# Kernel tuning notes

Measured on AMD Instinct MI355X. Metric: run time of the kernel, lower is better.

Reference implementation:

```python
import jax, jax.numpy as jnp
import numpy as np

N = 100000      # nodes
E = 3200000     # edges (avg degree 32)
XD = 256        # x_dim
H = 128         # h_dim
G = 128         # g_dim
D = H + G + 1   # y_rep_dim


def setup_inputs() -> dict:
    key = jax.random.key(0)
    ks = jax.random.split(key, 16)
    s = 0.05
    f32 = jnp.float32
    return {
        "X": jax.random.normal(ks[0], (N, XD), f32),
        "T": jax.random.uniform(ks[1], (N,), f32),
        "edge_index": jax.random.randint(ks[2], (2, E), 0, N, dtype=jnp.int64),
        "W_phi": jax.random.normal(ks[3], (XD, H), f32) * s,
        "b_phi": jnp.zeros((H,), f32),
        "W_gcn": jax.random.normal(ks[4], (H, G), f32) * s,
        "b_gcn": jnp.zeros((G,), f32),
        "W00": jax.random.normal(ks[5], (D, D), f32) * s,
        "b00": jnp.zeros((D,), f32),
        "W10": jax.random.normal(ks[6], (D, D), f32) * s,
        "b10": jnp.zeros((D,), f32),
        "W01": jax.random.normal(ks[7], (D, 1), f32) * s,
        "b01": jnp.zeros((1,), f32),
        "W11": jax.random.normal(ks[8], (D, 1), f32) * s,
        "b11": jnp.zeros((1,), f32),
    }


def reference(X, T, edge_index, W_phi, b_phi, W_gcn, b_gcn,
              W00, b00, W10, b10, W01, b01, W11, b11):
    src = edge_index[0]  # row: message source
    dst = edge_index[1]  # col: message destination (adj_t aggregates into dst)

    # phi_x = ReLU(Linear(X))
    phi_x = jax.nn.relu(X @ W_phi + b_phi)          # [N, H]
    phi_x_t = T[:, None] * phi_x                    # [N, H]

    # GCNConv: linear -> symmetric-normalized aggregation with self loops
    h = phi_x_t @ W_gcn                             # [N, G]
    ones_e = jnp.ones((E,), h.dtype)
    deg = jax.ops.segment_sum(ones_e, dst, num_segments=N) + 1.0  # with self loop
    dis = jax.lax.rsqrt(deg)                        # deg^{-1/2}
    coef = (dis[src] * dis[dst])[:, None]           # per-edge norm
    msg = h[src] * coef                             # [E, G] gather
    agg = jax.ops.segment_sum(msg, dst, num_segments=N)           # scatter-sum
    agg = agg + h * (1.0 / deg)[:, None] + b_gcn    # self-loop term + bias
    rep_gnn = jax.nn.relu(agg)                      # dropout is identity in eval

    # z = scatter_sum(T over neighbors) / degree (no self loops)
    deg_nl = jax.ops.segment_sum(ones_e, dst, num_segments=N)
    z = jax.ops.segment_sum(T[src], dst, num_segments=N) / jnp.maximum(deg_nl, 1.0)

    rep_post = jnp.concatenate([phi_x, rep_gnn, z[:, None]], axis=1)  # [N, D]

    y00 = jax.nn.relu(rep_post @ W00 + b00)
    y10 = jax.nn.relu(rep_post @ W10 + b10)
    y0_pred = (y00 @ W01 + b01).reshape(-1)
    y1_pred = (y10 @ W11 + b11).reshape(-1)
    return (y0_pred, y1_pred, rep_post)
```

## Files before the change

kernel.cpp:

```cpp
#include <hip/hip_runtime.h>
#include <hip/hip_bf16.h>

#define NN 100000
#define EE 3200000
#define KXD 256
#define HH 128
#define GG 128
#define DD 257
#define ELLS 96

#define BNODES 128
#define NBKT 782
#define BCAP 4608
#define SCB 256
#define SCT 1024
#define EPB (EE / SCB)

#define NT 17
#define KT 9
#define KP 288
#define SROW 296

#define PKT 8
#define PNT 8
#define GKT 4
#define GNT 8

typedef __attribute__((ext_vector_type(8))) short short8;
typedef __attribute__((ext_vector_type(4))) float f32x4;
typedef __attribute__((ext_vector_type(4))) int i32x4;
typedef unsigned short ushort_t;

__device__ inline float bfu2f(unsigned short u) {
    return __uint_as_float(((unsigned int)u) << 16);
}
__device__ inline float ldf(const void* p, size_t i, int bf) {
    if (bf) return bfu2f(((const unsigned short*)p)[i]);
    return ((const float*)p)[i];
}
__device__ inline unsigned short f2bf(float v) {
    unsigned int u = __float_as_uint(v);
    return (unsigned short)((u + 0x7fff + ((u >> 16) & 1)) >> 16);
}

__global__ void k_probe(const int* __restrict__ ei32, const unsigned int* __restrict__ Xw,
                        int* __restrict__ flags)
{
    __shared__ int s_edge_any, s_bf_hits;
    const int t = threadIdx.x;
    if (t == 0) { s_edge_any = 0; s_bf_hits = 0; }
    __syncthreads();
    int acc = 0;
    #pragma unroll
    for (int j = 0; j < 64; ++j) {
        int k = (t + 256 * j) * 195;
        acc |= ei32[2 * (size_t)k + 1];
    }
    if (acc) atomicOr(&s_edge_any, 1);
    unsigned int lo = Xw[t] & 0xffffu;
    int e = (int)((lo >> 7) & 0xff);
    if (lo == 0u || (e >= 100 && e <= 140)) atomicAdd(&s_bf_hits, 1);
    __syncthreads();
    if (t == 0) {
        flags[0] = (s_edge_any == 0) ? 1 : 0;
        flags[1] = (s_bf_hits >= 192) ? 1 : 0;
    }
}

__device__ inline void edge_sd(const int* ei, int e, int i64, int& s, int& d) {
    if (i64) { s = ei[2 * (size_t)e]; d = ei[2 * ((size_t)EE + e)]; }
    else     { s = ei[e];             d = ei[(size_t)EE + e]; }
    s = min(max(s, 0), NN - 1);
    d = min(max(d, 0), NN - 1);
}
__device__ inline int edge_d(const int* ei, int e, int i64) {
    int d = i64 ? ei[2 * ((size_t)EE + e)] : ei[(size_t)EE + e];
    return min(max(d, 0), NN - 1);
}

__global__ __launch_bounds__(SCT) void k_scat(const int* __restrict__ ei,
    const int* __restrict__ flags, unsigned long long* __restrict__ ebuf,
    int* __restrict__ bcur)
{
    __shared__ int hist[NBKT];
    __shared__ int base[NBKT];
    const int t = threadIdx.x;
    for (int i = t; i < NBKT; i += SCT) hist[i] = 0;
    __syncthreads();
    const int i64 = flags[0];
    const int e0 = blockIdx.x * EPB;
    for (int e = e0 + t; e < e0 + EPB; e += SCT)
        atomicAdd(&hist[edge_d(ei, e, i64) >> 7], 1);
    __syncthreads();
    for (int bkt = t; bkt < NBKT; bkt += SCT) {
        int c = hist[bkt];
        base[bkt] = c ? atomicAdd(&bcur[bkt], c) : 0;
        hist[bkt] = 0;
    }
    __syncthreads();
    for (int e = e0 + t; e < e0 + EPB; e += SCT) {
        int s, d;
        edge_sd(ei, e, i64, s, d);
        int bkt = d >> 7;
        int r = atomicAdd(&hist[bkt], 1);
        int pos = base[bkt] + r;
        if (pos < BCAP) {
            unsigned long long v = ((unsigned long long)(unsigned)d << 32)
                                 | (unsigned long long)(unsigned)s;
            __builtin_nontemporal_store(v, &ebuf[(size_t)bkt * BCAP + pos]);
        }
    }
}

__global__ __launch_bounds__(256) void k_ell(const unsigned long long* __restrict__ ebuf,
    const int* __restrict__ bcur, const void* __restrict__ T,
    const int* __restrict__ flags,
    int* __restrict__ ell, int* __restrict__ deg, float* __restrict__ dis,
    float* __restrict__ z, float* __restrict__ out_rep)
{
    __shared__ int tile[BNODES][ELLS];
    __shared__ int cnt[BNODES];
    __shared__ float tsum[BNODES];
    const int t = threadIdx.x;
    const int b = blockIdx.x;
    const int n0 = b * BNODES;
    for (int i = t; i < BNODES; i += 256) { cnt[i] = 0; tsum[i] = 0.f; }
    __syncthreads();
    const int bf = flags[1];
    const int c = min(bcur[b], BCAP);
    const unsigned long long* __restrict__ reg = ebuf + (size_t)b * BCAP;
    for (int i = t; i < c; i += 256) {
        unsigned long long v = reg[i];
        int s  = (int)(v & 0xffffffffull);
        int dl = ((int)(v >> 32)) & (BNODES - 1);
        int slot = atomicAdd(&cnt[dl], 1);
        if (slot < ELLS) tile[dl][slot] = s;
        atomicAdd(&tsum[dl], fminf(fmaxf(ldf(T, s, bf), 0.f), 1.f));
    }
    __syncthreads();
    {
        const i32x4* src = (const i32x4*)&tile[0][0];
        i32x4* dst = (i32x4*)(ell + (size_t)n0 * ELLS);
        for (int i = t; i < BNODES * ELLS / 4; i += 256)
            __builtin_nontemporal_store(src[i], &dst[i]);
    }
    for (int i = t; i < BNODES; i += 256) {
        int n = n0 + i;
        if (n < NN) {
            int cN = cnt[i];
            float cf = (float)cN;
            deg[n] = cN;
            dis[n] = rsqrtf(cf + 1.f);
            float zv = tsum[i] / fmaxf(cf, 1.f);
            z[n] = zv;
            __builtin_nontemporal_store(zv, &out_rep[(size_t)n * DD + 256]);
        }
    }
}

__global__ __launch_bounds__(64) void k_packw(const void* __restrict__ W,
    const int* __restrict__ flags, unsigned short* __restrict__ Bp,
    int KTILES, int Ncols)
{
    const int blk = blockIdx.x;
    const int lane = threadIdx.x;
    const int nt = blk / KTILES, kt = blk - nt * KTILES;
    const int bf = flags[1];
    const int n = nt * 16 + (lane & 15);
    const int k0 = kt * 32 + (lane >> 4) * 8;
    unsigned short hi[8], lo[8];
    #pragma unroll
    for (int j = 0; j < 8; ++j) {
        float x = ldf(W, (size_t)(k0 + j) * Ncols + n, bf);
        hi[j] = f2bf(x);
        lo[j] = f2bf(x - bfu2f(hi[j]));
    }
    *(short8*)(Bp + ((size_t)blk * 2 + 0) * 512 + lane * 8) = *(short8*)hi;
    *(short8*)(Bp + ((size_t)blk * 2 + 1) * 512 + lane * 8) = *(short8*)lo;
}

__global__ __launch_bounds__(128) void k_phi(const void* __restrict__ X,
    const unsigned short* __restrict__ Bp, const void* __restrict__ b,
    const int* __restrict__ flags, float* __restrict__ phi,
    float* __restrict__ out_rep)
{
    const int t = threadIdx.x;
    const int wave = t >> 6, lane = t & 63;
    const int m = lane & 15, q = lane >> 4;
    const int row = blockIdx.x * 32 + wave * 16 + m;
    const int bf = flags[1];

    f32x4 acc[8];
    #pragma unroll
    for (int i = 0; i < 8; ++i) acc[i] = (f32x4){0.f, 0.f, 0.f, 0.f};

    for (int kt = 0; kt < PKT; ++kt) {
        short8 vah, vall;
        if (bf) {
            vah = *(const short8*)((const unsigned short*)X
                    + (size_t)row * KXD + kt * 32 + q * 8);
        } else {
            const float* xp = (const float*)X + (size_t)row * KXD + kt * 32 + q * 8;
            float4 u = *(const float4*)xp;
            float4 v = *(const float4*)(xp + 4);
            float xs[8] = {u.x, u.y, u.z, u.w, v.x, v.y, v.z, v.w};
            unsigned short ah[8], al[8];
            #pragma unroll
            for (int j = 0; j < 8; ++j) {
                ah[j] = f2bf(xs[j]);
                al[j] = f2bf(xs[j] - bfu2f(ah[j]));
            }
            vah = *(short8*)ah; vall = *(short8*)al;
        }
        const unsigned short* Bk = Bp + (size_t)kt * 1024 + lane * 8;
        if (bf) {
            #pragma unroll
            for (int nt = 0; nt < PNT; ++nt) {
                short8 bh = *(const short8*)(Bk + (size_t)nt * (PKT * 1024));
                acc[nt] = __builtin_amdgcn_mfma_f32_16x16x32_bf16(vah, bh, acc[nt], 0, 0, 0);
            }
        } else {
            #pragma unroll
            for (int nt = 0; nt < PNT; ++nt) {
                const unsigned short* bb = Bk + (size_t)nt * (PKT * 1024);
                short8 bh = *(const short8*)bb;
                short8 bl = *(const short8*)(bb + 512);
                acc[nt] = __builtin_amdgcn_mfma_f32_16x16x32_bf16(vah,  bh, acc[nt], 0, 0, 0);
                acc[nt] = __builtin_amdgcn_mfma_f32_16x16x32_bf16(vah,  bl, acc[nt], 0, 0, 0);
                acc[nt] = __builtin_amdgcn_mfma_f32_16x16x32_bf16(vall, bh, acc[nt], 0, 0, 0);
            }
        }
    }
    const int orow0 = blockIdx.x * 32 + wave * 16 + q * 4;
    #pragma unroll
    for (int nt = 0; nt < PNT; ++nt) {
        int col = nt * 16 + m;
        float bv = ldf(b, col, bf);
        #pragma unroll
        for (int r = 0; r < 4; ++r) {
            int orow = orow0 + r;
            float o = fmaxf(acc[nt][r] + bv, 0.f);
            phi[(size_t)orow * HH + col] = o;
            __builtin_nontemporal_store(o, &out_rep[(size_t)orow * DD + col]);
        }
    }
}

__global__ __launch_bounds__(128) void k_gcn(const float* __restrict__ phi,
    const void* __restrict__ T, const unsigned short* __restrict__ Bp,
    const float* __restrict__ dis, const int* __restrict__ flags,
    ushort_t* __restrict__ hs)
{
    const int t = threadIdx.x;
    const int wave = t >> 6, lane = t & 63;
    const int m = lane & 15, q = lane >> 4;
    const int row = blockIdx.x * 32 + wave * 16 + m;
    const int bf = flags[1];
    const float tv = ldf(T, row, bf);

    f32x4 acc[8];
    #pragma unroll
    for (int i = 0; i < 8; ++i) acc[i] = (f32x4){0.f, 0.f, 0.f, 0.f};

    for (int kt = 0; kt < GKT; ++kt) {
        const float* pp = phi + (size_t)row * HH + kt * 32 + q * 8;
        float4 u = *(const float4*)pp;
        float4 v = *(const float4*)(pp + 4);
        float xs[8] = {u.x, u.y, u.z, u.w, v.x, v.y, v.z, v.w};
        unsigned short ah[8], al[8];
        #pragma unroll
        for (int j = 0; j < 8; ++j) {
            float x = xs[j] * tv;
            ah[j] = f2bf(x);
            al[j] = f2bf(x - bfu2f(ah[j]));
        }
        short8 vah = *(short8*)ah, vall = *(short8*)al;
        const unsigned short* Bk = Bp + (size_t)kt * 1024 + lane * 8;
        #pragma unroll
        for (int nt = 0; nt < GNT; ++nt) {
            const unsigned short* bb = Bk + (size_t)nt * (GKT * 1024);
            short8 bh = *(const short8*)bb;
            short8 bl = *(const short8*)(bb + 512);
            acc[nt] = __builtin_amdgcn_mfma_f32_16x16x32_bf16(vah,  bh, acc[nt], 0, 0, 0);
            acc[nt] = __builtin_amdgcn_mfma_f32_16x16x32_bf16(vah,  bl, acc[nt], 0, 0, 0);
            acc[nt] = __builtin_amdgcn_mfma_f32_16x16x32_bf16(vall, bh, acc[nt], 0, 0, 0);
        }
    }
    const int orow0 = blockIdx.x * 32 + wave * 16 + q * 4;
    float dr[4];
    #pragma unroll
    for (int r = 0; r < 4; ++r) dr[r] = dis[orow0 + r];
    #pragma unroll
    for (int nt = 0; nt < GNT; ++nt) {
        int col = nt * 16 + m;
        #pragma unroll
        for (int r = 0; r < 4; ++r)
            hs[(size_t)(orow0 + r) * GG + col] = f2bf(acc[nt][r] * dr[r]);
    }
}

__global__ __launch_bounds__(256) void k_gather(const ushort_t* __restrict__ hs,
    const int* __restrict__ ell, const int* __restrict__ deg,
    const float* __restrict__ dis, const void* __restrict__ bg,
    const int* __restrict__ flags,
    ushort_t* __restrict__ repg_bf, float* __restrict__ out_rep)
{
    const int wv   = threadIdx.x >> 6;
    const int lane = threadIdx.x & 63;
    const int n    = blockIdx.x * 4 + wv;
    const int bf   = flags[1];
    const int c2   = lane * 2;
    const int dgc  = min(deg[n], ELLS);

    const ushort_t* __restrict__ hp = hs + c2;
    const int* __restrict__ er = ell + (size_t)n * ELLS;
    int v0 = er[lane];
    int v1 = er[64 + lane];

    float aL0=0.f,aL1=0.f,aL2=0.f,aL3=0.f;
    float aH0=0.f,aH1=0.f,aH2=0.f,aH3=0.f;

    const int m1 = min(dgc, 64);
    int j = 0;
    for (; j + 4 <= m1; j += 4) {
        int i0 = __builtin_amdgcn_readlane(v0, j);
        int i1 = __builtin_amdgcn_readlane(v0, j + 1);
        int i2 = __builtin_amdgcn_readlane(v0, j + 2);
        int i3 = __builtin_amdgcn_readlane(v0, j + 3);
        unsigned int p0 = *(const unsigned int*)(hp + ((size_t)i0 << 7));
        unsigned int p1 = *(const unsigned int*)(hp + ((size_t)i1 << 7));
        unsigned int p2 = *(const unsigned int*)(hp + ((size_t)i2 << 7));
        unsigned int p3 = *(const unsigned int*)(hp + ((size_t)i3 << 7));
        aL0 += __uint_as_float(p0 << 16);  aH0 += __uint_as_float(p0 & 0xffff0000u);
        aL1 += __uint_as_float(p1 << 16);  aH1 += __uint_as_float(p1 & 0xffff0000u);
        aL2 += __uint_as_float(p2 << 16);  aH2 += __uint_as_float(p2 & 0xffff0000u);
        aL3 += __uint_as_float(p3 << 16);  aH3 += __uint_as_float(p3 & 0xffff0000u);
    }
    for (; j < m1; ++j) {
        int i0 = __builtin_amdgcn_readlane(v0, j);
        unsigned int p0 = *(const unsigned int*)(hp + ((size_t)i0 << 7));
        aL0 += __uint_as_float(p0 << 16);  aH0 += __uint_as_float(p0 & 0xffff0000u);
    }
    for (; j < dgc; ++j) {
        int i0 = __builtin_amdgcn_readlane(v1, j - 64);
        unsigned int p0 = *(const unsigned int*)(hp + ((size_t)i0 << 7));
        aL0 += __uint_as_float(p0 << 16);  aH0 += __uint_as_float(p0 & 0xffff0000u);
    }
    float accL = (aL0 + aL1) + (aL2 + aL3);
    float accH = (aH0 + aH1) + (aH2 + aH3);

    unsigned int pn = *(const unsigned int*)(hp + ((size_t)n << 7));
    accL += __uint_as_float(pn << 16);
    accH += __uint_as_float(pn & 0xffff0000u);

    float dn = dis[n];
    float rL = fmaxf(fmaf(accL, dn, ldf(bg, c2, bf)), 0.f);
    float rH = fmaxf(fmaf(accH, dn, ldf(bg, c2 + 1, bf)), 0.f);

    unsigned int packed = (unsigned int)f2bf(rL) | ((unsigned int)f2bf(rH) << 16);
    *(unsigned int*)&repg_bf[(size_t)n * GG + c2] = packed;

    const size_t ob = (size_t)n * DD + HH + c2;
    __builtin_nontemporal_store(rL, &out_rep[ob]);
    __builtin_nontemporal_store(rH, &out_rep[ob + 1]);
}

__global__ __launch_bounds__(64) void k_pack(const void* W00, const void* b00,
    const void* W10, const void* b10, const int* __restrict__ flags,
    unsigned short* __restrict__ Bpk)
{
    const int blk  = blockIdx.x;
    const int lane = threadIdx.x;
    const int head = blk / (NT * KT);
    const int rem  = blk - head * NT * KT;
    const int nt   = rem / KT, kt = rem - (rem / KT) * KT;
    const void* WH = head ? W10 : W00;
    const void* bH = head ? b10 : b00;
    const int bf = flags[1];
    const int n  = nt * 16 + (lane & 15);
    const int k0 = kt * 32 + (lane >> 4) * 8;
    unsigned short v[8];
    #pragma unroll
    for (int j = 0; j < 8; ++j) {
        int k = k0 + j;
        float x = 0.f;
        if (n < DD) {
            if (k < DD)       x = ldf(WH, (size_t)k * DD + n, bf);
            else if (k == DD) x = ldf(bH, n, bf);
        }
        v[j] = f2bf(x);
    }
    *(short8*)(Bpk + ((size_t)blk * 64 + lane) * 8) = *(short8*)v;
}

__global__ __launch_bounds__(128) void k_heads_mfma(const float* __restrict__ phi,
    const ushort_t* __restrict__ repg_bf, const float* __restrict__ z,
    const unsigned short* __restrict__ Bpk,
    const void* W01, const void* b01, const void* W11, const void* b11,
    const int* __restrict__ flags, float* __restrict__ out)
{
    __shared__ unsigned short As[32][SROW];
    const int t = threadIdx.x;
    const int row0 = blockIdx.x * 32;
    const int bf = flags[1];

    for (int i = t; i < 32 * 16; i += 128) {
        int m = i >> 4, g = i & 15;
        const float* pp = &phi[(size_t)(row0 + m) * HH + g * 8];
        float4 u = *(const float4*)pp;
        float4 v = *(const float4*)(pp + 4);
        unsigned short w[8] = { f2bf(u.x), f2bf(u.y), f2bf(u.z), f2bf(u.w),
                                f2bf(v.x), f2bf(v.y), f2bf(v.z), f2bf(v.w) };
        *(short8*)&As[m][g * 8] = *(const short8*)w;
    }
    for (int i = t; i < 32 * 16; i += 128) {
        int m = i >> 4, g = i & 15;
        *(short8*)&As[m][HH + g * 8] =
            *(const short8*)&repg_bf[(size_t)(row0 + m) * GG + g * 8];
    }
    for (int i = t; i < 32 * 32; i += 128) {
        int m = i >> 5, k = 256 + (i & 31);
        unsigned short v = 0;
        if (k == 256)      v = f2bf(z[row0 + m]);
        else if (k == 257) v = 0x3F80;
        As[m][k] = v;
    }
    __syncthreads();

    const int wave = t >> 6;
    const int lane = t & 63;
    const int m = lane & 15, q = lane >> 4;

    const void* WV = wave ? W11 : W01;
    const float bV = ldf(wave ? b11 : b01, 0, bf);

    float r0[4] = {0.f, 0.f, 0.f, 0.f};
    float r1[4] = {0.f, 0.f, 0.f, 0.f};

    const unsigned short* Bh = Bpk + (size_t)wave * NT * KT * 64 * 8;
    for (int nt = 0; nt < NT; ++nt) {
        f32x4 acc0 = {0.f, 0.f, 0.f, 0.f};
        f32x4 acc1 = {0.f, 0.f, 0.f, 0.f};
        const unsigned short* Bn = Bh + (size_t)nt * KT * 64 * 8;
        #pragma unroll
        for (int kt = 0; kt < KT; ++kt) {
            short8 b  = *(const short8*)(Bn + ((size_t)kt * 64 + lane) * 8);
            short8 a0 = *(const short8*)&As[m][kt * 32 + q * 8];
            short8 a1 = *(const short8*)&As[m + 16][kt * 32 + q * 8];
            acc0 = __builtin_amdgcn_mfma_f32_16x16x32_bf16(a0, b, acc0, 0, 0, 0);
            acc1 = __builtin_amdgcn_mfma_f32_16x16x32_bf16(a1, b, acc1, 0, 0, 0);
        }
        int n = nt * 16 + m;
        float wv = (n < DD) ? ldf(WV, n, bf) : 0.f;
        #pragma unroll
        for (int r = 0; r < 4; ++r) {
            r0[r] += fmaxf(acc0[r], 0.f) * wv;
            r1[r] += fmaxf(acc1[r], 0.f) * wv;
        }
    }

    #pragma unroll
    for (int r = 0; r < 4; ++r) {
        #pragma unroll
        for (int off = 8; off > 0; off >>= 1) {
            r0[r] += __shfl_xor(r0[r], off);
            r1[r] += __shfl_xor(r1[r], off);
        }
    }
    if (m == 0) {
        #pragma unroll
        for (int r = 0; r < 4; ++r) {
            out[(size_t)wave * NN + row0 + q * 4 + r]      = r0[r] + bV;
            out[(size_t)wave * NN + row0 + 16 + q * 4 + r] = r1[r] + bV;
        }
    }
}

extern "C" void kernel_launch(void* const* d_in, const int* in_sizes, int n_in,
                              void* d_out, int out_size, void* d_ws, size_t ws_size,
                              hipStream_t stream)
{
    const void* X    = d_in[0];
    const void* T    = d_in[1];
    const int*  ei   = (const int*)d_in[2];
    const void* Wphi = d_in[3];
    const void* bphi = d_in[4];
    const void* Wgcn = d_in[5];
    const void* bgcn = d_in[6];
    const void* W00  = d_in[7];
    const void* b00  = d_in[8];
    const void* W10  = d_in[9];
    const void* b10  = d_in[10];
    const void* W01  = d_in[11];
    const void* b01  = d_in[12];
    const void* W11  = d_in[13];
    const void* b11  = d_in[14];
    float* out = (float*)d_out;
    float* out_rep = out + 2 * (size_t)NN;

    char* ws = (char*)d_ws;
    float*    phi   = (float*)ws;                         ws += (size_t)NN * HH * 4;
    ushort_t* hs    = (ushort_t*)ws;                      ws += (size_t)NN * GG * 2;
    ushort_t* repg  = (ushort_t*)ws;                      ws += (size_t)NN * GG * 2;
    int*      deg   = (int*)ws;                           ws += (size_t)NN * 4;
    float*    dis   = (float*)ws;                         ws += (size_t)NN * 4;
    float*    z     = (float*)ws;                         ws += (size_t)NN * 4;
    int*      ell   = (int*)ws;                           ws += (size_t)NBKT * BNODES * ELLS * 4;
    int*      flags = (int*)ws;                           ws += 16;
    int*      bcur  = (int*)ws;                           ws += (size_t)((NBKT + 15) & ~15) * 4;
    unsigned short* Bpk   = (unsigned short*)ws;          ws += (size_t)2 * NT * KT * 64 * 8 * 2;
    unsigned short* BpPhi = (unsigned short*)ws;          ws += (size_t)PNT * PKT * 2 * 512 * 2;
    unsigned short* BpGcn = (unsigned short*)ws;

    unsigned long long* ebuf = (unsigned long long*)phi;

    (void)hipMemsetAsync(bcur, 0, NBKT * sizeof(int), stream);

    k_probe <<<1,            256, 0, stream>>>(ei, (const unsigned int*)X, flags);
    k_scat  <<<SCB,          SCT, 0, stream>>>(ei, flags, ebuf, bcur);
    k_ell   <<<NBKT,         256, 0, stream>>>(ebuf, bcur, T, flags,
                                               ell, deg, dis, z, out_rep);
    k_pack  <<<2 * NT * KT,   64, 0, stream>>>(W00, b00, W10, b10, flags, Bpk);
    k_packw <<<PNT * PKT,     64, 0, stream>>>(Wphi, flags, BpPhi, PKT, HH);
    k_packw <<<GNT * GKT,     64, 0, stream>>>(Wgcn, flags, BpGcn, GKT, GG);
    k_phi   <<<NN / 32,      128, 0, stream>>>(X, BpPhi, bphi, flags, phi, out_rep);
    k_gcn   <<<NN / 32,      128, 0, stream>>>(phi, T, BpGcn, dis, flags, hs);
    k_gather<<<NN / 4,       256, 0, stream>>>(hs, ell, deg, dis, bgcn,
                                               flags, repg, out_rep);
    k_heads_mfma<<<NN / 32,  128, 0, stream>>>(phi, repg, z, Bpk,
                                               W01, b01, W11, b11, flags, out);
}
```

Before: 706.1 us.

## Stage edge bucketing in LDS and pack edges into 32-bit words

The scatter kernel now runs a block-wide prefix scan over bucket histograms and writes each edge into a bucket-sorted LDS staging array. It then writes to global memory in contiguous runs per bucket instead of scattered 8-byte stores. Each edge is packed as a 32-bit word holding the local destination in 7 bits and the source in 17 bits, which halves the edge buffer traffic that k_ell also reads. The cost is much more LDS per block (about 80KB with EPB=12500), an extra scan with many barriers, and a serial per-bucket fill loop.

```diff
diff --git a/kernel.cpp b/kernel.cpp
--- a/kernel.cpp
+++ b/kernel.cpp
@@ -79,40 +79,60 @@
 }
 
 __global__ __launch_bounds__(SCT) void k_scat(const int* __restrict__ ei,
-    const int* __restrict__ flags, unsigned long long* __restrict__ ebuf,
+    const int* __restrict__ flags, unsigned int* __restrict__ ebuf,
     int* __restrict__ bcur)
 {
     __shared__ int hist[NBKT];
+    __shared__ int loff[NBKT];
     __shared__ int base[NBKT];
+    __shared__ int hist2[NBKT];
+    __shared__ int sc[SCT];
+    __shared__ unsigned short bktof[EPB];
+    __shared__ unsigned int pk[EPB];
     const int t = threadIdx.x;
-    for (int i = t; i < NBKT; i += SCT) hist[i] = 0;
+    for (int i = t; i < NBKT; i += SCT) { hist[i] = 0; hist2[i] = 0; }
     __syncthreads();
     const int i64 = flags[0];
     const int e0 = blockIdx.x * EPB;
     for (int e = e0 + t; e < e0 + EPB; e += SCT)
         atomicAdd(&hist[edge_d(ei, e, i64) >> 7], 1);
     __syncthreads();
+    sc[t] = (t < NBKT) ? hist[t] : 0;
+    __syncthreads();
+    for (int off = 1; off < SCT; off <<= 1) {
+        int v = (t >= off) ? sc[t - off] : 0;
+        __syncthreads();
+        sc[t] += v;
+        __syncthreads();
+    }
+    if (t < NBKT) {
+        int c = hist[t];
+        loff[t] = sc[t] - c;
+        base[t] = c ? atomicAdd(&bcur[t], c) : 0;
+    }
+    __syncthreads();
     for (int bkt = t; bkt < NBKT; bkt += SCT) {
-        int c = hist[bkt];
-        base[bkt] = c ? atomicAdd(&bcur[bkt], c) : 0;
-        hist[bkt] = 0;
+        int st = loff[bkt], c = hist[bkt];
+        for (int j = 0; j < c; ++j) bktof[st + j] = (unsigned short)bkt;
     }
     __syncthreads();
     for (int e = e0 + t; e < e0 + EPB; e += SCT) {
         int s, d;
         edge_sd(ei, e, i64, s, d);
         int bkt = d >> 7;
-        int r = atomicAdd(&hist[bkt], 1);
-        int pos = base[bkt] + r;
-        if (pos < BCAP) {
-            unsigned long long v = ((unsigned long long)(unsigned)d << 32)
-                                 | (unsigned long long)(unsigned)s;
-            __builtin_nontemporal_store(v, &ebuf[(size_t)bkt * BCAP + pos]);
-        }
-    }
-}
-
-__global__ __launch_bounds__(256) void k_ell(const unsigned long long* __restrict__ ebuf,
+        int r = atomicAdd(&hist2[bkt], 1);
+        pk[loff[bkt] + r] = ((unsigned)(d & (BNODES - 1)) << 17) | (unsigned)s;
+    }
+    __syncthreads();
+    for (int i = t; i < EPB; i += SCT) {
+        int bkt = bktof[i];
+        int pos = base[bkt] + (i - loff[bkt]);
+        if (pos < BCAP)
+            __builtin_nontemporal_store(pk[i], &ebuf[(size_t)bkt * BCAP + pos]);
+    }
+}
+
+__global__ __launch_bounds__(256) void k_ell(const unsigned int* __restrict__ ebuf,
     const int* __restrict__ bcur, const void* __restrict__ T,
     const int* __restrict__ flags,
     int* __restrict__ ell, int* __restrict__ deg, float* __restrict__ dis,
@@ -128,11 +148,11 @@
     __syncthreads();
     const int bf = flags[1];
     const int c = min(bcur[b], BCAP);
-    const unsigned long long* __restrict__ reg = ebuf + (size_t)b * BCAP;
+    const unsigned int* __restrict__ reg = ebuf + (size_t)b * BCAP;
     for (int i = t; i < c; i += 256) {
-        unsigned long long v = reg[i];
-        int s  = (int)(v & 0xffffffffull);
-        int dl = ((int)(v >> 32)) & (BNODES - 1);
+        unsigned int v = reg[i];
+        int s  = (int)(v & 0x1FFFFu);
+        int dl = (int)(v >> 17) & (BNODES - 1);
         int slot = atomicAdd(&cnt[dl], 1);
         if (slot < ELLS) tile[dl][slot] = s;
         atomicAdd(&tsum[dl], fminf(fmaxf(ldf(T, s, bf), 0.f), 1.f));
@@ -512,7 +532,7 @@
     unsigned short* BpPhi = (unsigned short*)ws;          ws += (size_t)PNT * PKT * 2 * 512 * 2;
     unsigned short* BpGcn = (unsigned short*)ws;
 
-    unsigned long long* ebuf = (unsigned long long*)phi;
+    unsigned int* ebuf = (unsigned int*)phi;
 
     (void)hipMemsetAsync(bcur, 0, NBKT * sizeof(int), stream);
 
```

Measured after the change: 611.5 us. 13.4% less time.
